# Kernel optimization log

Measured on AMD Instinct MI355X. Metric: run time of the kernel, lower is better.

## Reference

```python
import jax, jax.numpy as jnp
import numpy as np

B, TS, TD = 32, 64, 63          # batch, src len, dec steps (dm_max_length_chinese-1)
VS, VT = 32000, 32000           # source/target vocab
E, U = 256, 1024                # embed dim, LSTM units


def _lstm_step(x_t, h, c, Wx, Wh, b):
    # Keras gate order: i, f, g(candidate), o
    z = x_t @ Wx + h @ Wh + b                      # [B, 4U]
    i, f, g, o = jnp.split(z, 4, axis=-1)
    c_new = jax.nn.sigmoid(f) * c + jax.nn.sigmoid(i) * jnp.tanh(g)
    h_new = jax.nn.sigmoid(o) * jnp.tanh(c_new)
    return h_new, c_new


def setup_inputs() -> dict:
    key = jax.random.key(0)
    ks = jax.random.split(key, 16)
    s_e = 1.0 / np.sqrt(E)
    s_u = 1.0 / np.sqrt(U)
    s_eu = 1.0 / np.sqrt(E + U)
    return {
        "encoder_input": jax.random.randint(ks[0], (B, TS), 0, VS, dtype=jnp.int32),
        "decoder_input": jax.random.randint(ks[1], (B, TD), 0, VT, dtype=jnp.int32),
        "enc_emb": jax.random.normal(ks[2], (VS, E), jnp.float32) * 0.02,
        "dec_emb": jax.random.normal(ks[3], (VT, E), jnp.float32) * 0.02,
        "Wx_e": jax.random.normal(ks[4], (E, 4 * U), jnp.float32) * s_e,
        "Wh_e": jax.random.normal(ks[5], (U, 4 * U), jnp.float32) * s_u,
        "b_e": jnp.zeros((4 * U,), jnp.float32),
        "Wx_d": jax.random.normal(ks[6], (E + U, 4 * U), jnp.float32) * s_eu,
        "Wh_d": jax.random.normal(ks[7], (U, 4 * U), jnp.float32) * s_u,
        "b_d": jnp.zeros((4 * U,), jnp.float32),
        "Wm": jax.random.normal(ks[8], (U, U), jnp.float32) * s_u,    # Luong memory layer (no bias)
        "Wa": jax.random.normal(ks[9], (2 * U, U), jnp.float32) * (1.0 / np.sqrt(2 * U)),  # attention layer (no bias)
        "Wf": jax.random.normal(ks[10], (U, VT), jnp.float32) * s_u,
        "bf": jnp.zeros((VT,), jnp.float32),
    }


def reference(encoder_input, decoder_input, enc_emb, dec_emb,
              Wx_e, Wh_e, b_e, Wx_d, Wh_d, b_d, Wm, Wa, Wf, bf):
    # ---- Encoder: Embedding + LSTM(return_sequences, return_state) ----
    enc_x = enc_emb[encoder_input]                          # [B, TS, E]

    def enc_step(carry, x_t):
        h, c = carry
        h, c = _lstm_step(x_t, h, c, Wx_e, Wh_e, b_e)
        return (h, c), h

    h0 = jnp.zeros((B, U), enc_x.dtype)
    (h_enc, c_enc), memory = jax.lax.scan(enc_step, (h0, h0),
                                          jnp.swapaxes(enc_x, 0, 1))
    memory = jnp.swapaxes(memory, 0, 1)                     # [B, TS, U]

    # Luong attention keys: memory_layer(memory)
    keys = jnp.einsum('bsu,uv->bsv', memory, Wm)            # [B, TS, U]

    # ---- Decoder: AttentionWrapper(LSTMCell) + output Dense, per step ----
    dec_x = dec_emb[decoder_input]                          # [B, TD, E]

    def dec_step(carry, x_t):
        h, c, attn = carry
        cell_in = jnp.concatenate([x_t, attn], axis=-1)     # [B, E+U]
        h, c = _lstm_step(cell_in, h, c, Wx_d, Wh_d, b_d)
        score = jnp.einsum('bu,bsu->bs', h, keys)           # Luong dot score
        align = jax.nn.softmax(score, axis=-1)              # full-length mask -> plain softmax
        context = jnp.einsum('bs,bsu->bu', align, memory)
        attn = jnp.concatenate([h, context], axis=-1) @ Wa  # attention layer, no bias
        logits = attn @ Wf + bf                             # output projection
        return (h, c, attn), logits

    attn0 = jnp.zeros((B, U), dec_x.dtype)
    _, logits = jax.lax.scan(dec_step, (h_enc, c_enc, attn0),
                             jnp.swapaxes(dec_x, 0, 1))
    return jnp.swapaxes(logits, 0, 1)                       # [B, TD, VT]
```

## Files before the change

kernel.cpp:

```cpp
#include <hip/hip_runtime.h>
#include <hip/hip_bf16.h>

#define B_  32
#define TS_ 64
#define TD_ 63
#define E_  256
#define U_  1024
#define G_  4096
#define VT_ 32000

typedef __attribute__((ext_vector_type(8))) short short8;
typedef __attribute__((ext_vector_type(4))) float floatx4;

__device__ __forceinline__ float sigf(float x){ return 1.0f/(1.0f+__expf(-x)); }
__device__ __forceinline__ float tanh_fast(float x){ return 2.0f/(1.0f+__expf(-2.0f*x)) - 1.0f; }
__device__ __forceinline__ unsigned short f2bf(float x){
  unsigned u = __float_as_uint(x);
  u += 0x7FFFu + ((u>>16)&1u);
  return (unsigned short)(u>>16);
}

__global__ void zero_kernel(float4* __restrict__ p, int n4){
  int i = blockIdx.x*256 + threadIdx.x;
  if(i < n4) p[i] = make_float4(0.f,0.f,0.f,0.f);
}

__global__ __launch_bounds__(256) void gemm_rows(
    const float* __restrict__ Atab, const int* __restrict__ tokens, int T,
    const float* __restrict__ Bw, const float* __restrict__ bias,
    float* __restrict__ C, int N, int K)
{
  __shared__ float as[64*20];
  int tid = threadIdx.x;
  int n  = blockIdx.x*256 + tid;
  int m0 = blockIdx.y*16;
  float acc[16];
  #pragma unroll
  for(int r=0;r<16;r++) acc[r]=0.f;

  for(int kc=0; kc<K; kc+=64){
    __syncthreads();
    for(int i=tid; i<16*64; i+=256){
      int mm = i>>6, kk = i&63;
      int m = m0 + mm;
      const float* arow;
      if(tokens){
        int b = m & 31, t = m >> 5;
        arow = Atab + (size_t)tokens[b*T + t]*K;
      } else {
        arow = Atab + (size_t)m*K;
      }
      as[kk*20 + mm] = arow[kc + kk];
    }
    __syncthreads();
    for(int kk=0; kk<64; kk++){
      float bv = Bw[(size_t)(kc+kk)*N + n];
      const float4* ap = (const float4*)(as + kk*20);
      float4 a0 = ap[0], a1 = ap[1], a2 = ap[2], a3 = ap[3];
      acc[0]  += a0.x*bv; acc[1]  += a0.y*bv; acc[2]  += a0.z*bv; acc[3]  += a0.w*bv;
      acc[4]  += a1.x*bv; acc[5]  += a1.y*bv; acc[6]  += a1.z*bv; acc[7]  += a1.w*bv;
      acc[8]  += a2.x*bv; acc[9]  += a2.y*bv; acc[10] += a2.z*bv; acc[11] += a2.w*bv;
      acc[12] += a3.x*bv; acc[13] += a3.y*bv; acc[14] += a3.z*bv; acc[15] += a3.w*bv;
    }
  }
  float bv = bias ? bias[n] : 0.f;
  #pragma unroll
  for(int r=0;r<16;r++)
    C[(size_t)(m0+r)*N + n] = acc[r] + bv;
}

__global__ __launch_bounds__(256) void step_mm(
    const float* __restrict__ W1, const float* __restrict__ W2,
    const float* __restrict__ s1, const float* __restrict__ s2,
    float* __restrict__ zpart, int N, int HQ)
{
  int tid = threadIdx.x;
  int lane = tid & 63, mg = tid >> 6;
  int n = blockIdx.x*64 + lane;
  int kq = blockIdx.y;
  const float* W;
  const float* hp;
  if(kq < HQ){
    int k0 = kq*128;
    W  = W1 + (size_t)k0*N + n;
    hp = s1 + (size_t)(mg*8)*U_ + k0;
  } else {
    int k0 = (kq-HQ)*128;
    W  = W2 + (size_t)k0*N + n;
    hp = s2 + (size_t)(mg*8)*U_ + k0;
  }
  float acc[8];
  #pragma unroll
  for(int i=0;i<8;i++) acc[i]=0.f;

  for(int kk=0; kk<128; kk+=16){
    float w[16];
    #pragma unroll
    for(int j=0;j<16;j++) w[j] = W[(size_t)(kk+j)*N];
    #pragma unroll
    for(int mi=0; mi<8; mi++){
      const float4* h4 = (const float4*)(hp + (size_t)mi*U_ + kk);
      float4 ha = h4[0], hb = h4[1], hc = h4[2], hd = h4[3];
      acc[mi] += ha.x*w[0]  + ha.y*w[1]  + ha.z*w[2]  + ha.w*w[3]
               + hb.x*w[4]  + hb.y*w[5]  + hb.z*w[6]  + hb.w*w[7]
               + hc.x*w[8]  + hc.y*w[9]  + hc.z*w[10] + hc.w*w[11]
               + hd.x*w[12] + hd.y*w[13] + hd.z*w[14] + hd.w*w[15];
    }
  }
  float* zp = zpart + ((size_t)(kq*32 + mg*8)) * N + n;
  #pragma unroll
  for(int mi=0; mi<8; mi++)
    zp[(size_t)mi * N] = acc[mi];
}

__global__ __launch_bounds__(256) void gate_h(
    const float* __restrict__ X_t, const float* __restrict__ zpart, int KQ,
    float* __restrict__ c, float* __restrict__ hout)
{
  int i = blockIdx.x*256 + threadIdx.x;
  int b = i >> 10, u = i & 1023;
  float zg[4];
  #pragma unroll
  for(int g=0; g<4; g++){
    int col = g*U_ + u;
    float s = X_t[(size_t)b*G_ + col];
    for(int p=0; p<KQ; p++) s += zpart[((size_t)(p*32+b))*G_ + col];
    zg[g] = s;
  }
  float cn = sigf(zg[1])*c[i] + sigf(zg[0])*tanh_fast(zg[2]);
  float hn = sigf(zg[3])*tanh_fast(cn);
  c[i] = cn;
  hout[i] = hn;
}

__global__ __launch_bounds__(256) void dec_gate_attn(
    const float* __restrict__ Xd_t, const float* __restrict__ zpart,
    float* __restrict__ c, const float* __restrict__ keys,
    const float* __restrict__ memory, float* __restrict__ hout,
    float* __restrict__ ctx)
{
  int b = blockIdx.x;
  int tid = threadIdx.x;
  __shared__ float hs[1024];
  __shared__ float sc[64];
  __shared__ float al[64];
  #pragma unroll
  for(int uu=0; uu<4; uu++){
    int u = uu*256 + tid;
    float zg[4];
    #pragma unroll
    for(int g=0; g<4; g++){
      int col = g*U_ + u;
      float s = Xd_t[(size_t)b*G_ + col];
      #pragma unroll
      for(int p=0; p<16; p++) s += zpart[((size_t)(p*32+b))*G_ + col];
      zg[g] = s;
    }
    int ci = b*U_ + u;
    float cn = sigf(zg[1])*c[ci] + sigf(zg[0])*tanh_fast(zg[2]);
    float hn = sigf(zg[3])*tanh_fast(cn);
    c[ci] = cn;
    hs[u] = hn;
    hout[ci] = hn;
  }
  __syncthreads();
  int w = tid>>6, lane = tid&63;
  for(int si=0; si<16; si++){
    int s = w*16 + si;
    const float* kr = keys + ((size_t)s*B_ + b)*U_;
    float p = 0.f;
    for(int kk=lane; kk<1024; kk+=64) p += hs[kk]*kr[kk];
    for(int off=32; off; off>>=1) p += __shfl_down(p, off);
    if(lane==0) sc[s] = p;
  }
  __syncthreads();
  if(tid<64){
    float v = sc[tid];
    float mx = v;
    for(int off=32; off; off>>=1) mx = fmaxf(mx, __shfl_down(mx, off));
    mx = __shfl(mx, 0);
    float e = __expf(v - mx);
    float sm = e;
    for(int off=32; off; off>>=1) sm += __shfl_down(sm, off);
    sm = __shfl(sm, 0);
    al[tid] = e/sm;
  }
  __syncthreads();
  #pragma unroll
  for(int uu=0; uu<4; uu++){
    int u = uu*256 + tid;
    float a = 0.f;
    for(int s=0; s<64; s++) a += al[s]*memory[((size_t)s*B_ + b)*U_ + u];
    ctx[b*U_ + u] = a;
  }
}

__global__ __launch_bounds__(256) void attn_combine(
    const float* __restrict__ apart, float* __restrict__ attn_next,
    unsigned short* __restrict__ abf)
{
  int i = blockIdx.x*256 + threadIdx.x;
  float s = 0.f;
  #pragma unroll
  for(int p=0; p<16; p++) s += apart[(size_t)p*32768 + i];
  attn_next[i] = s;
  abf[i] = f2bf(s);
}

__global__ __launch_bounds__(256) void transpose_f2bf(
    const float* __restrict__ Wf, unsigned short* __restrict__ WfT)
{
  __shared__ float t[32][33];
  int n0 = blockIdx.x*32, k0 = blockIdx.y*32;
  int tid = threadIdx.x;
  int cx = tid&31, ry = tid>>5;
  for(int r=ry; r<32; r+=8) t[r][cx] = Wf[(size_t)(k0+r)*VT_ + n0+cx];
  __syncthreads();
  for(int r=ry; r<32; r+=8)
    WfT[(size_t)(n0+r)*1024 + k0+cx] = f2bf(t[cx][r]);
}

__global__ __launch_bounds__(256) void logits_gemm(
    const unsigned short* __restrict__ Abf, const unsigned short* __restrict__ Bt,
    const float* __restrict__ bias, float* __restrict__ out)
{
  __shared__ __align__(16) unsigned short As[32][40];
  __shared__ __align__(16) unsigned short Bs[256][40];
  int tid = threadIdx.x;
  int m0 = blockIdx.x*32, n0 = blockIdx.y*256;
  int w = tid>>6, lane = tid&63;
  int wm = w&1, wn = w>>1;
  floatx4 acc[8];
  #pragma unroll
  for(int i=0;i<8;i++) acc[i] = (floatx4)(0.f);

  int rl = lane&15, kg = lane>>4;

  for(int kt=0; kt<1024; kt+=32){
    __syncthreads();
    {
      int mm = tid>>3, kq = tid&7;
      const unsigned short* src = Abf + (size_t)(m0+mm)*1024 + kt + kq*4;
      *(uint2*)(&As[mm][kq*4]) = *(const uint2*)src;
    }
    {
      const unsigned short* bsrc = Bt + (size_t)(n0+tid)*1024 + kt;
      *(uint4*)(&Bs[tid][0])  = *(const uint4*)(bsrc);
      *(uint4*)(&Bs[tid][8])  = *(const uint4*)(bsrc+8);
      *(uint4*)(&Bs[tid][16]) = *(const uint4*)(bsrc+16);
      *(uint4*)(&Bs[tid][24]) = *(const uint4*)(bsrc+24);
    }
    __syncthreads();
    short8 afrag = *(const short8*)(&As[wm*16 + rl][kg*8]);
    #pragma unroll
    for(int nt=0; nt<8; nt++){
      short8 bfrag = *(const short8*)(&Bs[wn*128 + nt*16 + rl][kg*8]);
      acc[nt] = __builtin_amdgcn_mfma_f32_16x16x32_bf16(afrag, bfrag, acc[nt], 0,0,0);
    }
  }
  #pragma unroll
  for(int nt=0; nt<8; nt++){
    int n = n0 + wn*128 + nt*16 + rl;
    float bv = bias[n];
    #pragma unroll
    for(int r=0;r<4;r++){
      int m = m0 + wm*16 + kg*4 + r;
      int t = m>>5, b = m&31;
      out[((size_t)(b*TD_) + t)*VT_ + n] = acc[nt][r] + bv;
    }
  }
}

extern "C" void kernel_launch(void* const* d_in, const int* in_sizes, int n_in,
                              void* d_out, int out_size, void* d_ws, size_t ws_size,
                              hipStream_t stream) {
  (void)in_sizes; (void)n_in; (void)out_size; (void)ws_size;
  const int*   enc_in  = (const int*)d_in[0];
  const int*   dec_in  = (const int*)d_in[1];
  const float* enc_emb = (const float*)d_in[2];
  const float* dec_emb = (const float*)d_in[3];
  const float* Wx_e    = (const float*)d_in[4];
  const float* Wh_e    = (const float*)d_in[5];
  const float* b_e     = (const float*)d_in[6];
  const float* Wx_d    = (const float*)d_in[7];
  const float* Wh_d    = (const float*)d_in[8];
  const float* b_d     = (const float*)d_in[9];
  const float* Wm      = (const float*)d_in[10];
  const float* Wa      = (const float*)d_in[11];
  const float* Wf      = (const float*)d_in[12];
  const float* bf      = (const float*)d_in[13];
  float* out = (float*)d_out;

  float* ws = (float*)d_ws;
  size_t off = 0;
  float* Xe       = ws + off; off += (size_t)TS_*B_*G_;
  float* Xd       = ws + off; off += (size_t)TD_*B_*G_;
  float* memory   = ws + off; off += (size_t)TS_*B_*U_;
  float* keys     = ws + off; off += (size_t)TS_*B_*U_;
  float* attn_buf = ws + off; off += (size_t)64*B_*U_;
  float* cbuf     = ws + off; off += (size_t)B_*U_;
  float* hbuf     = ws + off; off += (size_t)B_*U_;
  float* ctx      = ws + off; off += (size_t)B_*U_;
  float* zpart    = ws + off; off += (size_t)16*B_*G_;
  float* apart    = ws + off; off += (size_t)16*B_*U_;
  unsigned short* attn_bf = (unsigned short*)(ws + off); off += (size_t)(2016*1024)/2;
  unsigned short* WfT     = (unsigned short*)(ws + off);

  zero_kernel<<<32, 256, 0, stream>>>((float4*)attn_buf, (B_*U_)/4);
  zero_kernel<<<32, 256, 0, stream>>>((float4*)cbuf, (B_*U_)/4);

  gemm_rows<<<dim3(G_/256, (TS_*B_)/16), 256, 0, stream>>>(enc_emb, enc_in, TS_, Wx_e, b_e, Xe, G_, E_);
  gemm_rows<<<dim3(G_/256, (TD_*B_)/16), 256, 0, stream>>>(dec_emb, dec_in, TD_, Wx_d, b_d, Xd, G_, E_);
  transpose_f2bf<<<dim3(VT_/32, 1024/32), 256, 0, stream>>>(Wf, WfT);

  for(int t=0; t<TS_; t++){
    const float* hprev = (t==0) ? attn_buf : memory + (size_t)(t-1)*B_*U_;
    step_mm<<<dim3(G_/64, 8), 256, 0, stream>>>(Wh_e, Wh_e, hprev, hprev, zpart, G_, 8);
    gate_h<<<128, 256, 0, stream>>>(Xe + (size_t)t*B_*G_, zpart, 8, cbuf,
                                    memory + (size_t)t*B_*U_);
  }

  gemm_rows<<<dim3(U_/256, (TS_*B_)/16), 256, 0, stream>>>(memory, nullptr, 0, Wm, nullptr, keys, U_, U_);

  const float* mem_last = memory + (size_t)(TS_-1)*B_*U_;
  const float* Wxa = Wx_d + (size_t)E_*G_;
  const float* Wa2 = Wa + (size_t)U_*U_;
  for(int t=0; t<TD_; t++){
    const float* hin   = (t==0) ? mem_last : hbuf;
    const float* aprev = attn_buf + (size_t)t*B_*U_;
    float* anext       = attn_buf + (size_t)(t+1)*B_*U_;
    step_mm<<<dim3(G_/64, 16), 256, 0, stream>>>(Wh_d, Wxa, hin, aprev, zpart, G_, 8);
    dec_gate_attn<<<B_, 256, 0, stream>>>(Xd + (size_t)t*B_*G_, zpart, cbuf,
                                          keys, memory, hbuf, ctx);
    step_mm<<<dim3(U_/64, 16), 256, 0, stream>>>(Wa, Wa2, hbuf, ctx, apart, U_, 8);
    attn_combine<<<128, 256, 0, stream>>>(apart, anext, attn_bf + (size_t)t*B_*U_);
  }

  logits_gemm<<<dim3((TD_*B_)/32, VT_/256), 256, 0, stream>>>(attn_bf, WfT, bf, out);
}
```

Before: 16.01 ms.

## Replace per-step RNN kernel launches with persistent cooperative kernels and grid barriers

The encoder and decoder recurrences become two persistent cooperative kernels of 512 blocks each, synchronised by a hand-written atomic grid barrier, instead of 2–4 kernel launches per time step. Recurrent weights are pre-transposed so each thread reads a contiguous weight row for its dot products, and the whole decoder step (gates, attention, attention layer) runs inside the kernel. This is meant to remove launch overhead and inter-kernel gaps across about 190 sequential steps. In exchange it adds extra transposes, a large workspace requirement, and reliance on cooperative-launch residency, with the old launch path kept as a fallback.

After: 29.44 ms. 84.0% more time.

```diff
diff --git a/kernel.cpp b/kernel.cpp
--- a/kernel.cpp
+++ b/kernel.cpp
@@ -8,6 +8,7 @@
 #define U_  1024
 #define G_  4096
 #define VT_ 32000
+#define NB_ 512
 
 typedef __attribute__((ext_vector_type(8))) short short8;
 typedef __attribute__((ext_vector_type(4))) float floatx4;
@@ -18,6 +19,28 @@
   unsigned u = __float_as_uint(x);
   u += 0x7FFFu + ((u>>16)&1u);
   return (unsigned short)(u>>16);
+}
+
+__device__ __forceinline__ void st_wt(float* p, float v){
+  __hip_atomic_store(p, v, __ATOMIC_RELAXED, __HIP_MEMORY_SCOPE_AGENT);
+}
+
+__device__ __forceinline__ void gbar_sync(unsigned* bar, unsigned n){
+  asm volatile("s_waitcnt vmcnt(0)" ::: "memory");
+  __syncthreads();
+  if(threadIdx.x==0){
+    int g = blockIdx.x >> 4;
+    unsigned v = __hip_atomic_fetch_add(bar + g*32, 1u, __ATOMIC_RELAXED, __HIP_MEMORY_SCOPE_AGENT);
+    if((v & 15u) == 15u){
+      unsigned r = __hip_atomic_fetch_add(bar + 1024, 1u, __ATOMIC_RELAXED, __HIP_MEMORY_SCOPE_AGENT);
+      if((r & 31u) == 31u)
+        __hip_atomic_store(bar + 1056, n, __ATOMIC_RELAXED, __HIP_MEMORY_SCOPE_AGENT);
+    }
+    while(__hip_atomic_load(bar + 1056, __ATOMIC_RELAXED, __HIP_MEMORY_SCOPE_AGENT) < n)
+      __builtin_amdgcn_s_sleep(1);
+  }
+  __syncthreads();
+  asm volatile("" ::: "memory");
 }
 
 __global__ void zero_kernel(float4* __restrict__ p, int n4){
@@ -67,6 +90,187 @@
   #pragma unroll
   for(int r=0;r<16;r++)
     C[(size_t)(m0+r)*N + n] = acc[r] + bv;
+}
+
+__global__ __launch_bounds__(256) void transpose_f32(
+    const float* __restrict__ src, float* __restrict__ dst,
+    int N, int dstStride, int dstOff)
+{
+  __shared__ float tle[32][33];
+  int n0 = blockIdx.x*32, k0 = blockIdx.y*32;
+  int tid = threadIdx.x, cx = tid&31, ry = tid>>5;
+  for(int r=ry; r<32; r+=8) tle[r][cx] = src[(size_t)(k0+r)*N + n0+cx];
+  __syncthreads();
+  for(int r=ry; r<32; r+=8)
+    dst[(size_t)(n0+r)*dstStride + dstOff + k0+cx] = tle[cx][r];
+}
+
+struct EncP {
+  const float* WheT; const float* Xe; const float* zeros;
+  float* memory; float* cst; unsigned* bar;
+};
+__global__ __launch_bounds__(256, 2) void enc_rnn(EncP P)
+{
+  const int bid = blockIdx.x, tid = threadIdx.x;
+  const int x = bid & 7, j = bid >> 3;
+  const int cg = x*16 + (j>>2), bq = j & 3;
+  const int u0 = cg*8;
+  const int bL = tid & 7, lc = tid >> 3;
+  const int b  = bq*8 + bL;
+  const int col = (lc>>3)*U_ + u0 + (lc&7);
+  const float4* wrow = (const float4*)(P.WheT + (size_t)col*U_);
+  const int gb = tid & 7, gu = tid >> 3;
+  const int gB = bq*8 + gb, gU = u0 + gu;
+  __shared__ float zs[32][8];
+  float c_reg = 0.f;
+  unsigned bc = 0;
+
+  for(int t=0; t<TS_; t++){
+    const float* hsrc = t ? (P.memory + (size_t)(t-1)*B_*U_) : P.zeros;
+    const float4* hv = (const float4*)(hsrc + (size_t)b*U_);
+    float acc = 0.f;
+    #pragma unroll 8
+    for(int k=0; k<U_/4; k++){
+      float4 h4 = hv[k], w4 = wrow[k];
+      acc += h4.x*w4.x + h4.y*w4.y + h4.z*w4.z + h4.w*w4.w;
+    }
+    zs[lc][bL] = acc;
+    __syncthreads();
+    if(tid < 64){
+      const float* Xt = P.Xe + (size_t)t*B_*G_ + (size_t)gB*G_;
+      float zi = Xt[gU]        + zs[gu][gb];
+      float zf = Xt[U_+gU]     + zs[8+gu][gb];
+      float zg = Xt[2*U_+gU]   + zs[16+gu][gb];
+      float zo = Xt[3*U_+gU]   + zs[24+gu][gb];
+      float cn = sigf(zf)*c_reg + sigf(zi)*tanh_fast(zg);
+      float hn = sigf(zo)*tanh_fast(cn);
+      c_reg = cn;
+      st_wt(P.memory + (size_t)t*B_*U_ + (size_t)gB*U_ + gU, hn);
+    }
+    gbar_sync(P.bar, ++bc);
+  }
+  if(tid < 64) P.cst[(size_t)gB*U_ + gU] = c_reg;
+}
+
+struct DecP {
+  const float* WdT; const float* WaT; const float* Xd;
+  const float* keys; const float* memory; const float* h_enc;
+  float* hdec; float* ctxb; float* attn; const float* cst;
+  unsigned short* attn_bf; unsigned* bar;
+};
+__global__ __launch_bounds__(256, 2) void dec_rnn(DecP P)
+{
+  const int bid = blockIdx.x, tid = threadIdx.x;
+  const int x = bid & 7, j = bid >> 3;
+  const int cg = x*16 + (j>>2), bq = j & 3;
+  const int u0 = cg*8;
+  const int bL = tid & 7, lc = tid >> 3;
+  const int b  = bq*8 + bL;
+  const int col = (lc>>3)*U_ + u0 + (lc&7);
+  const float4* wrow = (const float4*)(P.WdT + (size_t)col*2048);
+  const int gb = tid & 7, gu = tid >> 3;
+  const int gB = bq*8 + gb, gU = u0 + gu;
+  const int d3 = tid >> 2, part = tid & 3;
+  const int b3 = bq*8 + (d3 & 7), c3 = cg*8 + (d3 >> 3);
+  const float4* warow = (const float4*)(P.WaT + (size_t)c3*2048);
+  __shared__ float zs[32][8];
+  __shared__ float hs[1024];
+  __shared__ float sc[64];
+  __shared__ float al[64];
+  float c_reg = 0.f;
+  if(tid < 64) c_reg = P.cst[(size_t)gB*U_ + gU];
+  unsigned bc = 0;
+
+  for(int t=0; t<TD_; t++){
+    {
+      const float* hsrc = t ? (P.hdec + (size_t)(t-1)*B_*U_) : P.h_enc;
+      const float* asrc = P.attn + (size_t)t*B_*U_;
+      const float4* hv = (const float4*)(hsrc + (size_t)b*U_);
+      const float4* av = (const float4*)(asrc + (size_t)b*U_);
+      float acc = 0.f;
+      #pragma unroll 8
+      for(int k=0; k<256; k++){
+        float4 h4 = hv[k], w4 = wrow[k];
+        acc += h4.x*w4.x + h4.y*w4.y + h4.z*w4.z + h4.w*w4.w;
+      }
+      #pragma unroll 8
+      for(int k=0; k<256; k++){
+        float4 a4 = av[k], w4 = wrow[256+k];
+        acc += a4.x*w4.x + a4.y*w4.y + a4.z*w4.z + a4.w*w4.w;
+      }
+      zs[lc][bL] = acc;
+      __syncthreads();
+      if(tid < 64){
+        const float* Xt = P.Xd + (size_t)t*B_*G_ + (size_t)gB*G_;
+        float zi = Xt[gU]        + zs[gu][gb];
+        float zf = Xt[U_+gU]     + zs[8+gu][gb];
+        float zg = Xt[2*U_+gU]   + zs[16+gu][gb];
+        float zo = Xt[3*U_+gU]   + zs[24+gu][gb];
+        float cn = sigf(zf)*c_reg + sigf(zi)*tanh_fast(zg);
+        float hn = sigf(zo)*tanh_fast(cn);
+        c_reg = cn;
+        st_wt(P.hdec + (size_t)t*B_*U_ + (size_t)gB*U_ + gU, hn);
+      }
+    }
+    gbar_sync(P.bar, ++bc);
+    if(bid < B_){
+      const int bb = bid;
+      const float* hrow = P.hdec + (size_t)t*B_*U_ + (size_t)bb*U_;
+      for(int i=tid; i<1024; i+=256) hs[i] = hrow[i];
+      __syncthreads();
+      int w = tid>>6, ln = tid&63;
+      for(int si=0; si<16; si++){
+        int s = w*16 + si;
+        const float* kr = P.keys + ((size_t)s*B_ + bb)*U_;
+        float p = 0.f;
+        for(int kk=ln; kk<1024; kk+=64) p += hs[kk]*kr[kk];
+        #pragma unroll
+        for(int off=32; off; off>>=1) p += __shfl_down(p, off);
+        if(ln==0) sc[s] = p;
+      }
+      __syncthreads();
+      if(tid < 64){
+        float v = sc[tid], mx = v;
+        #pragma unroll
+        for(int off=32; off; off>>=1) mx = fmaxf(mx, __shfl_down(mx, off));
+        mx = __shfl(mx, 0);
+        float e = __expf(v - mx), sm = e;
+        #pragma unroll
+        for(int off=32; off; off>>=1) sm += __shfl_down(sm, off);
+        sm = __shfl(sm, 0);
+        al[tid] = e/sm;
+      }
+      __syncthreads();
+      #pragma unroll
+      for(int uu=0; uu<4; uu++){
+        int u = uu*256 + tid;
+        float a = 0.f;
+        for(int s=0; s<64; s++) a += al[s]*P.memory[((size_t)s*B_ + bb)*U_ + u];
+        st_wt(P.ctxb + (size_t)t*B_*U_ + (size_t)bb*U_ + u, a);
+      }
+    }
+    gbar_sync(P.bar, ++bc);
+    {
+      const float* hsrc = P.hdec + (size_t)t*B_*U_ + (size_t)b3*U_;
+      const float* csrc = P.ctxb + (size_t)t*B_*U_ + (size_t)b3*U_;
+      const float4* sv = (part < 2) ? (const float4*)hsrc : (const float4*)csrc;
+      const int sbase = (part & 1)*128;
+      const float4* wv = warow + part*128;
+      float acc = 0.f;
+      #pragma unroll 8
+      for(int i=0; i<128; i++){
+        float4 s4 = sv[sbase+i], w4 = wv[i];
+        acc += s4.x*w4.x + s4.y*w4.y + s4.z*w4.z + s4.w*w4.w;
+      }
+      acc += __shfl_xor(acc, 1);
+      acc += __shfl_xor(acc, 2);
+      if(part == 0){
+        st_wt(P.attn + (size_t)(t+1)*B_*U_ + (size_t)b3*U_ + c3, acc);
+        P.attn_bf[(size_t)t*B_*U_ + (size_t)b3*U_ + c3] = f2bf(acc);
+      }
+    }
+    gbar_sync(P.bar, ++bc);
+  }
 }
 
 __global__ __launch_bounds__(256) void step_mm(
@@ -92,11 +296,10 @@
   float acc[8];
   #pragma unroll
   for(int i=0;i<8;i++) acc[i]=0.f;
-
   for(int kk=0; kk<128; kk+=16){
     float w[16];
     #pragma unroll
-    for(int j=0;j<16;j++) w[j] = W[(size_t)(kk+j)*N];
+    for(int jj=0;jj<16;jj++) w[jj] = W[(size_t)(kk+jj)*N];
     #pragma unroll
     for(int mi=0; mi<8; mi++){
       const float4* h4 = (const float4*)(hp + (size_t)mi*U_ + kk);
@@ -274,7 +477,7 @@
 extern "C" void kernel_launch(void* const* d_in, const int* in_sizes, int n_in,
                               void* d_out, int out_size, void* d_ws, size_t ws_size,
                               hipStream_t stream) {
-  (void)in_sizes; (void)n_in; (void)out_size; (void)ws_size;
+  (void)in_sizes; (void)n_in; (void)out_size;
   const int*   enc_in  = (const int*)d_in[0];
   const int*   dec_in  = (const int*)d_in[1];
   const float* enc_emb = (const float*)d_in[2];
@@ -298,42 +501,83 @@
   float* memory   = ws + off; off += (size_t)TS_*B_*U_;
   float* keys     = ws + off; off += (size_t)TS_*B_*U_;
   float* attn_buf = ws + off; off += (size_t)64*B_*U_;
-  float* cbuf     = ws + off; off += (size_t)B_*U_;
+  float* cst      = ws + off; off += (size_t)B_*U_;
   float* hbuf     = ws + off; off += (size_t)B_*U_;
-  float* ctx      = ws + off; off += (size_t)B_*U_;
+  float* ctxs     = ws + off; off += (size_t)B_*U_;
   float* zpart    = ws + off; off += (size_t)16*B_*G_;
   float* apart    = ws + off; off += (size_t)16*B_*U_;
   unsigned short* attn_bf = (unsigned short*)(ws + off); off += (size_t)(2016*1024)/2;
-  unsigned short* WfT     = (unsigned short*)(ws + off);
+  unsigned short* WfT     = (unsigned short*)(ws + off); off += (size_t)(VT_*1024)/2;
+  size_t coop_base = off;
+  float* WheT = ws + off; off += (size_t)G_*U_;
+  float* WdT  = ws + off; off += (size_t)G_*2048;
+  float* WaT  = ws + off; off += (size_t)U_*2048;
+  float* hdec = ws + off; off += (size_t)TD_*B_*U_;
+  float* ctxb = ws + off; off += (size_t)TD_*B_*U_;
+  unsigned* bar = (unsigned*)(ws + off); off += 2048;
+  size_t need_bytes = off * sizeof(float);
+  (void)coop_base;
+
+  bool coop_ok = (need_bytes <= ws_size);
 
   zero_kernel<<<32, 256, 0, stream>>>((float4*)attn_buf, (B_*U_)/4);
-  zero_kernel<<<32, 256, 0, stream>>>((float4*)cbuf, (B_*U_)/4);
+  zero_kernel<<<32, 256, 0, stream>>>((float4*)cst, (B_*U_)/4);
 
   gemm_rows<<<dim3(G_/256, (TS_*B_)/16), 256, 0, stream>>>(enc_emb, enc_in, TS_, Wx_e, b_e, Xe, G_, E_);
   gemm_rows<<<dim3(G_/256, (TD_*B_)/16), 256, 0, stream>>>(dec_emb, dec_in, TD_, Wx_d, b_d, Xd, G_, E_);
   transpose_f2bf<<<dim3(VT_/32, 1024/32), 256, 0, stream>>>(Wf, WfT);
 
-  for(int t=0; t<TS_; t++){
-    const float* hprev = (t==0) ? attn_buf : memory + (size_t)(t-1)*B_*U_;
-    step_mm<<<dim3(G_/64, 8), 256, 0, stream>>>(Wh_e, Wh_e, hprev, hprev, zpart, G_, 8);
-    gate_h<<<128, 256, 0, stream>>>(Xe + (size_t)t*B_*G_, zpart, 8, cbuf,
-                                    memory + (size_t)t*B_*U_);
-  }
-
-  gemm_rows<<<dim3(U_/256, (TS_*B_)/16), 256, 0, stream>>>(memory, nullptr, 0, Wm, nullptr, keys, U_, U_);
-
-  const float* mem_last = memory + (size_t)(TS_-1)*B_*U_;
   const float* Wxa = Wx_d + (size_t)E_*G_;
-  const float* Wa2 = Wa + (size_t)U_*U_;
-  for(int t=0; t<TD_; t++){
-    const float* hin   = (t==0) ? mem_last : hbuf;
-    const float* aprev = attn_buf + (size_t)t*B_*U_;
-    float* anext       = attn_buf + (size_t)(t+1)*B_*U_;
-    step_mm<<<dim3(G_/64, 16), 256, 0, stream>>>(Wh_d, Wxa, hin, aprev, zpart, G_, 8);
-    dec_gate_attn<<<B_, 256, 0, stream>>>(Xd + (size_t)t*B_*G_, zpart, cbuf,
-                                          keys, memory, hbuf, ctx);
-    step_mm<<<dim3(U_/64, 16), 256, 0, stream>>>(Wa, Wa2, hbuf, ctx, apart, U_, 8);
-    attn_combine<<<128, 256, 0, stream>>>(apart, anext, attn_bf + (size_t)t*B_*U_);
+
+  if(coop_ok){
+    zero_kernel<<<2, 256, 0, stream>>>((float4*)bar, 2048/4);
+    transpose_f32<<<dim3(128, 32), 256, 0, stream>>>(Wh_e, WheT, G_, U_, 0);
+    transpose_f32<<<dim3(128, 32), 256, 0, stream>>>(Wh_d, WdT, G_, 2048, 0);
+    transpose_f32<<<dim3(128, 32), 256, 0, stream>>>(Wxa,  WdT, G_, 2048, U_);
+    transpose_f32<<<dim3(32, 64),  256, 0, stream>>>(Wa,   WaT, U_, 2048, 0);
+
+    EncP ep;
+    ep.WheT = WheT; ep.Xe = Xe; ep.zeros = attn_buf;
+    ep.memory = memory; ep.cst = cst; ep.bar = bar;
+    void* ea[1] = { (void*)&ep };
+    hipError_t e1 = hipLaunchCooperativeKernel(enc_rnn, dim3(NB_), dim3(256), ea, 0u, stream);
+    if(e1 != hipSuccess) coop_ok = false;
+
+    if(coop_ok){
+      gemm_rows<<<dim3(U_/256, (TS_*B_)/16), 256, 0, stream>>>(memory, nullptr, 0, Wm, nullptr, keys, U_, U_);
+      DecP dp;
+      dp.WdT = WdT; dp.WaT = WaT; dp.Xd = Xd;
+      dp.keys = keys; dp.memory = memory; dp.h_enc = memory + (size_t)(TS_-1)*B_*U_;
+      dp.hdec = hdec; dp.ctxb = ctxb; dp.attn = attn_buf; dp.cst = cst;
+      dp.attn_bf = attn_bf; dp.bar = bar + 128;
+      void* da[1] = { (void*)&dp };
+      hipError_t e2 = hipLaunchCooperativeKernel(dec_rnn, dim3(NB_), dim3(256), da, 0u, stream);
+      if(e2 != hipSuccess) coop_ok = false;
+    }
+  }
+
+  if(!coop_ok){
+    zero_kernel<<<32, 256, 0, stream>>>((float4*)attn_buf, (B_*U_)/4);
+    zero_kernel<<<32, 256, 0, stream>>>((float4*)cst, (B_*U_)/4);
+    for(int t=0; t<TS_; t++){
+      const float* hprev = (t==0) ? attn_buf : memory + (size_t)(t-1)*B_*U_;
+      step_mm<<<dim3(G_/64, 8), 256, 0, stream>>>(Wh_e, Wh_e, hprev, hprev, zpart, G_, 8);
+      gate_h<<<128, 256, 0, stream>>>(Xe + (size_t)t*B_*G_, zpart, 8, cst,
+                                      memory + (size_t)t*B_*U_);
+    }
+    gemm_rows<<<dim3(U_/256, (TS_*B_)/16), 256, 0, stream>>>(memory, nullptr, 0, Wm, nullptr, keys, U_, U_);
+    const float* mem_last = memory + (size_t)(TS_-1)*B_*U_;
+    const float* Wa2 = Wa + (size_t)U_*U_;
+    for(int t=0; t<TD_; t++){
+      const float* hin   = (t==0) ? mem_last : hbuf;
+      const float* aprev = attn_buf + (size_t)t*B_*U_;
+      float* anext       = attn_buf + (size_t)(t+1)*B_*U_;
+      step_mm<<<dim3(G_/64, 16), 256, 0, stream>>>(Wh_d, Wxa, hin, aprev, zpart, G_, 8);
+      dec_gate_attn<<<B_, 256, 0, stream>>>(Xd + (size_t)t*B_*G_, zpart, cst,
+                                            keys, memory, hbuf, ctxs);
+      step_mm<<<dim3(U_/64, 16), 256, 0, stream>>>(Wa, Wa2, hbuf, ctxs, apart, U_, 8);
+      attn_combine<<<128, 256, 0, stream>>>(apart, anext, attn_bf + (size_t)t*B_*U_);
+    }
   }
 
   logits_gemm<<<dim3((TD_*B_)/32, VT_/256), 256, 0, stream>>>(attn_bf, WfT, bf, out);
```
